# Kernel optimization log

Measured on AMD Instinct MI355X. Metric: run time of the kernel, lower is better.

The kernel has to match this reference:

```python
import jax, jax.numpy as jnp
import numpy as np

INPUT_DIM = 512
N_TREES = 64
TREE_DEPTH = 3
N_LEAVES = 2 ** TREE_DEPTH      # 8
N_INTERNAL = 2 ** TREE_DEPTH - 1  # 7
PPT = N_INTERNAL * (INPUT_DIM + 1) + N_LEAVES * 2  # params per tree = 3607
BATCH = 65536


def setup_inputs() -> dict:
    key = jax.random.key(0)
    k1, k2, k3 = jax.random.split(key, 3)
    x = jax.random.normal(k1, (BATCH, INPUT_DIM), dtype=jnp.float32)
    tree_params = jax.random.normal(k2, (1, N_TREES * PPT), dtype=jnp.float32)
    tree_weights = jax.random.normal(k3, (1, N_TREES), dtype=jnp.float32)
    return {"x": x, "tree_params": tree_params, "tree_weights": tree_weights}


def reference(x, tree_params, tree_weights):
    # Unpack all trees at once: [T, ppt]
    p = tree_params[0].reshape(N_TREES, PPT)
    split_w = p[:, : N_INTERNAL * INPUT_DIM].reshape(N_TREES, N_INTERNAL, INPUT_DIM)
    split_b = p[:, N_INTERNAL * INPUT_DIM : N_INTERNAL * (INPUT_DIM + 1)]  # [T, I]
    leaf_logits = p[:, N_INTERNAL * (INPUT_DIM + 1) :].reshape(N_TREES, N_LEAVES, 2)

    # decisions: [B, T, I]
    decisions = jax.nn.sigmoid(jnp.einsum('bd,tid->bti', x, split_w) + split_b[None])

    # Replicate the original indexing quirk: leaf_probs column j (a tree NODE index)
    # gets factor d_i if j == 2i+1 (and j < n_leaves), (1-d_i) if j == 2i+2.
    # Column 0 remains 1.0; each other column gets exactly one factor.
    cols = []
    for j in range(N_LEAVES):
        if j == 0:
            cols.append(jnp.ones_like(decisions[:, :, 0]))
        elif j % 2 == 1:
            i = (j - 1) // 2
            cols.append(decisions[:, :, i] if i < N_INTERNAL else jnp.ones_like(decisions[:, :, 0]))
        else:
            i = (j - 2) // 2
            cols.append(1.0 - decisions[:, :, i] if i < N_INTERNAL else jnp.ones_like(decisions[:, :, 0]))
    leaf_probs = jnp.stack(cols, axis=-1)  # [B, T, L]
    leaf_probs = leaf_probs / (leaf_probs.sum(axis=-1, keepdims=True) + 1e-8)

    leaf_dist = jax.nn.softmax(leaf_logits, axis=-1)  # [T, L, 2]
    tree_out = jnp.einsum('btl,tlc->btc', leaf_probs, leaf_dist)  # [B, T, 2]
    return jnp.einsum('btc,t->bc', tree_out, tree_weights[0])  # [B, 2]
```

## Files before the change

kernel.cpp:

```cpp
#include <hip/hip_runtime.h>
#include <stdint.h>


#define KDIM 512
#define PPT 3607
#define NP 8
#define EPI_S 260
#define E_OFF 65536
#define P_OFF 98816
#define P_S 34
#define AB_OFF 103168
#define LDS_BYTES 105728

typedef _Float16 f16x8 __attribute__((ext_vector_type(8)));
typedef float f32x4 __attribute__((ext_vector_type(4)));

__global__ __launch_bounds__(128) void prep_kernel(const float* __restrict__ p,
                                                   const float* __restrict__ tw,
                                                   _Float16* __restrict__ Wh,
                                                   float* __restrict__ biasN,
                                                   float* __restrict__ AB) {
    const int c = blockIdx.x;
    const int t = c >> 2, i = c & 3;
    const float* wsrc = p + t * PPT + i * KDIM;
    for (int k = threadIdx.x; k < KDIM; k += 128)
        Wh[c * KDIM + k] = (_Float16)wsrc[k];
    if (threadIdx.x == 0)
        biasN[c] = p[t * PPT + 7 * KDIM + i];
    if (threadIdx.x == 64 && c < 64) {
        const int tt = c;
        const float* lg = p + tt * PPT + 7 * 513;
        const float w = tw[tt];
        float ld[8][2];
#pragma unroll
        for (int j = 0; j < 8; ++j) {
            float a = lg[2 * j], b = lg[2 * j + 1];
            float m = fmaxf(a, b);
            float e0 = expf(a - m), e1 = expf(b - m);
            float s = e0 + e1;
            ld[j][0] = e0 / s; ld[j][1] = e1 / s;
        }
        float* o = AB + tt * 10;
#pragma unroll
        for (int cc = 0; cc < 2; ++cc) {
            o[0 + cc] = w * (ld[0][cc] + ld[2][cc] + ld[4][cc] + ld[6][cc]);
            o[2 + cc] = w * (ld[1][cc] - ld[2][cc]);
            o[4 + cc] = w * (ld[3][cc] - ld[4][cc]);
            o[6 + cc] = w * (ld[5][cc] - ld[6][cc]);
            o[8 + cc] = w * (ld[7][cc]);
        }
    }
}

__device__ __forceinline__ f16x8 cvt8(float4 a, float4 b) {
    f16x8 h;
    h[0] = (_Float16)a.x; h[1] = (_Float16)a.y; h[2] = (_Float16)a.z; h[3] = (_Float16)a.w;
    h[4] = (_Float16)b.x; h[5] = (_Float16)b.y; h[6] = (_Float16)b.z; h[7] = (_Float16)b.w;
    return h;
}

__global__ __launch_bounds__(512, 2) void main_kernel(const float* __restrict__ X,
                                                      const _Float16* __restrict__ Wh,
                                                      const float* __restrict__ biasN,
                                                      const float* __restrict__ ABg,
                                                      float* __restrict__ out) {
    extern __shared__ char smem[];
    const int tid = threadIdx.x;
    const int lane = tid & 63;
    const int wn = tid >> 6;
    const int r15 = lane & 15;
    const int hi = lane >> 4;
    const int gr0 = blockIdx.x * 256;

    {
        float* abl = (float*)(smem + AB_OFF);
        for (int i = tid; i < 640; i += 512) abl[i] = ABg[i];
    }

    f16x8 Wf[16][2];
#pragma unroll
    for (int s = 0; s < 16; ++s)
#pragma unroll
        for (int ct = 0; ct < 2; ++ct)
            Wf[s][ct] = *(const f16x8*)&Wh[(size_t)(wn * 32 + ct * 16 + r15) * KDIM + s * 32 + hi * 8];

    float bl[2];
#pragma unroll
    for (int ct = 0; ct < 2; ++ct) bl[ct] = biasN[wn * 32 + ct * 16 + r15];

    int srow[4], ldw[4];
#pragma unroll
    for (int i = 0; i < 4; ++i) {
        int chunk = i * 512 + tid;
        int row = chunk >> 6, g = chunk & 63;
        srow[i] = chunk * 8;
        ldw[i] = row * 1024 + ((g ^ (row & 15)) << 4);
    }

    const int aoff0 = r15 * 1024;
    const int aoff1 = (16 + r15) * 1024;

    const float* Xblk = X + (size_t)gr0 * KDIM;
    float4 xr[8];

#pragma unroll
    for (int i = 0; i < 4; ++i) {
        xr[2 * i]     = *(const float4*)(Xblk + srow[i]);
        xr[2 * i + 1] = *(const float4*)(Xblk + srow[i] + 4);
    }

    for (int p = 0; p < NP; ++p) {
        char* xb = smem + (p & 1) * 32768;
#pragma unroll
        for (int i = 0; i < 4; ++i)
            *(f16x8*)(xb + ldw[i]) = cvt8(xr[2 * i], xr[2 * i + 1]);
        if (p + 1 < NP) {
            const float* Xp = Xblk + (size_t)(p + 1) * 32 * KDIM;
#pragma unroll
            for (int i = 0; i < 4; ++i) {
                xr[2 * i]     = *(const float4*)(Xp + srow[i]);
                xr[2 * i + 1] = *(const float4*)(Xp + srow[i] + 4);
            }
        }
        asm volatile("s_waitcnt lgkmcnt(0)" ::: "memory");
        __builtin_amdgcn_s_barrier();

        f32x4 acc[2][2];
#pragma unroll
        for (int rt = 0; rt < 2; ++rt)
#pragma unroll
            for (int ct = 0; ct < 2; ++ct)
                acc[rt][ct] = (f32x4){0.f, 0.f, 0.f, 0.f};
#pragma unroll
        for (int s = 0; s < 16; ++s) {
            const int go = ((s * 4 + hi) ^ r15) << 4;
            f16x8 a0 = *(const f16x8*)(xb + aoff0 + go);
            f16x8 a1 = *(const f16x8*)(xb + aoff1 + go);
            acc[0][0] = __builtin_amdgcn_mfma_f32_16x16x32_f16(a0, Wf[s][0], acc[0][0], 0, 0, 0);
            acc[0][1] = __builtin_amdgcn_mfma_f32_16x16x32_f16(a0, Wf[s][1], acc[0][1], 0, 0, 0);
            acc[1][0] = __builtin_amdgcn_mfma_f32_16x16x32_f16(a1, Wf[s][0], acc[1][0], 0, 0, 0);
            acc[1][1] = __builtin_amdgcn_mfma_f32_16x16x32_f16(a1, Wf[s][1], acc[1][1], 0, 0, 0);
        }

        float* Ef = (float*)(smem + E_OFF);
#pragma unroll
        for (int rt = 0; rt < 2; ++rt)
#pragma unroll
            for (int ct = 0; ct < 2; ++ct) {
                const int col = wn * 32 + ct * 16 + r15;
#pragma unroll
                for (int reg = 0; reg < 4; ++reg) {
                    const int row = rt * 16 + hi * 4 + reg;
                    float z = acc[rt][ct][reg] + bl[ct];
                    Ef[row * EPI_S + col] = __builtin_amdgcn_rcpf(1.f + __expf(-z));
                }
            }
        asm volatile("s_waitcnt lgkmcnt(0)" ::: "memory");
        __builtin_amdgcn_s_barrier();
        {
            const float* abl = (const float*)(smem + AB_OFF);
            float* Pf = (float*)(smem + P_OFF);
            const int row = tid >> 4, tg = tid & 15;
            float s0 = 0.f, s1 = 0.f;
#pragma unroll
            for (int j = 0; j < 4; ++j) {
                const int t = tg * 4 + j;
                float4 dv = *(const float4*)&Ef[row * EPI_S + t * 4];
                const float* abt = &abl[t * 10];
                float inv = __builtin_amdgcn_rcpf(4.f + dv.w + 1e-8f);
                s0 += (abt[0] + dv.x * abt[2] + dv.y * abt[4] + dv.z * abt[6] + dv.w * abt[8]) * inv;
                s1 += (abt[1] + dv.x * abt[3] + dv.y * abt[5] + dv.z * abt[7] + dv.w * abt[9]) * inv;
            }
            Pf[row * P_S + tg * 2 + 0] = s0;
            Pf[row * P_S + tg * 2 + 1] = s1;
        }
        asm volatile("s_waitcnt lgkmcnt(0)" ::: "memory");
        __builtin_amdgcn_s_barrier();
        if (tid < 64) {
            const float* Pf = (const float*)(smem + P_OFF);
            const int row = tid >> 1, c = tid & 1;
            float s = 0.f;
#pragma unroll
            for (int tg = 0; tg < 16; ++tg) s += Pf[row * P_S + tg * 2 + c];
            out[(size_t)(gr0 + p * 32 + row) * 2 + c] = s;
        }
    }
}

extern "C" void kernel_launch(void* const* d_in, const int* in_sizes, int n_in,
                              void* d_out, int out_size, void* d_ws, size_t ws_size,
                              hipStream_t stream) {
    const float* x  = (const float*)d_in[0];
    const float* tp = (const float*)d_in[1];
    const float* tw = (const float*)d_in[2];
    float* out = (float*)d_out;

    _Float16* Wh = (_Float16*)d_ws;
    float* biasN = (float*)((char*)d_ws + 262144);
    float* AB    = (float*)((char*)d_ws + 263168);

    (void)hipFuncSetAttribute((const void*)reinterpret_cast<const void*>(&main_kernel),
                              hipFuncAttributeMaxDynamicSharedMemorySize, LDS_BYTES);

    prep_kernel<<<256, 128, 0, stream>>>(tp, tw, Wh, biasN, AB);
    main_kernel<<<256, 512, LDS_BYTES, stream>>>(x, Wh, biasN, AB, out);
}
```

Before: 47.62 us.

## Restructure GEMM into K-streamed 128x256 block tiles with async weight staging

Instead of holding all weights in registers and streaming 32-row X panels, each block now computes a 128-row by 256-column tile by looping over K in 16-wide steps. Weights are staged through a triple-buffered LDS ring via global_load_lds, and X goes through a double-buffered fp16 LDS tile. The grid doubles to 512 blocks with a smaller LDS footprint, aiming for higher occupancy and better latency hiding. The cost is 32 barriers per block, use of the smaller 16x16x16 MFMA, and weights re-read from global memory by every block.

Result: slower. 51.27 us (+7.7%).

```diff
diff --git a/kernel.cpp b/kernel.cpp
--- a/kernel.cpp
+++ b/kernel.cpp
@@ -4,16 +4,10 @@
 
 #define KDIM 512
 #define PPT 3607
-#define NP 8
-#define EPI_S 260
-#define E_OFF 65536
-#define P_OFF 98816
-#define P_S 34
-#define AB_OFF 103168
-#define LDS_BYTES 105728
-
-typedef _Float16 f16x8 __attribute__((ext_vector_type(8)));
+
+typedef _Float16 f16x4 __attribute__((ext_vector_type(4)));
 typedef float f32x4 __attribute__((ext_vector_type(4)));
+
 
 __global__ __launch_bounds__(128) void prep_kernel(const float* __restrict__ p,
                                                    const float* __restrict__ tw,
@@ -52,14 +46,28 @@
     }
 }
 
-__device__ __forceinline__ f16x8 cvt8(float4 a, float4 b) {
-    f16x8 h;
-    h[0] = (_Float16)a.x; h[1] = (_Float16)a.y; h[2] = (_Float16)a.z; h[3] = (_Float16)a.w;
-    h[4] = (_Float16)b.x; h[5] = (_Float16)b.y; h[6] = (_Float16)b.z; h[7] = (_Float16)b.w;
+#define XB_STRIDE 5120
+#define WB0 10240
+#define WB_STRIDE 8192
+#define EPI_S 260
+#define P_OFF 66560
+#define P_S 18
+#define AB_OFF 71168
+#define LDS_BYTES 73728
+
+__device__ __forceinline__ void gll16(const void* g, void* l) {
+    __builtin_amdgcn_global_load_lds((const __attribute__((address_space(1))) uint32_t*)g,
+                                     (__attribute__((address_space(3))) uint32_t*)l, 16, 0, 0);
+}
+
+__device__ __forceinline__ f16x4 cvt4(float4 a) {
+    f16x4 h;
+    h[0] = (_Float16)a.x; h[1] = (_Float16)a.y;
+    h[2] = (_Float16)a.z; h[3] = (_Float16)a.w;
     return h;
 }
 
-__global__ __launch_bounds__(512, 2) void main_kernel(const float* __restrict__ X,
+__global__ __launch_bounds__(512, 4) void main_kernel(const float* __restrict__ X,
                                                       const _Float16* __restrict__ Wh,
                                                       const float* __restrict__ biasN,
                                                       const float* __restrict__ ABg,
@@ -67,104 +75,119 @@
     extern __shared__ char smem[];
     const int tid = threadIdx.x;
     const int lane = tid & 63;
-    const int wn = tid >> 6;
+    const int w = tid >> 6;
+    const int wm = w >> 2;
+    const int wn = w & 3;
     const int r15 = lane & 15;
     const int hi = lane >> 4;
-    const int gr0 = blockIdx.x * 256;
+    const int gr0 = blockIdx.x * 128;
 
     {
         float* abl = (float*)(smem + AB_OFF);
         for (int i = tid; i < 640; i += 512) abl[i] = ABg[i];
     }
-
-    f16x8 Wf[16][2];
-#pragma unroll
-    for (int s = 0; s < 16; ++s)
-#pragma unroll
-        for (int ct = 0; ct < 2; ++ct)
-            Wf[s][ct] = *(const f16x8*)&Wh[(size_t)(wn * 32 + ct * 16 + r15) * KDIM + s * 32 + hi * 8];
-
-    float bl[2];
-#pragma unroll
-    for (int ct = 0; ct < 2; ++ct) bl[ct] = biasN[wn * 32 + ct * 16 + r15];
-
-    int srow[4], ldw[4];
-#pragma unroll
-    for (int i = 0; i < 4; ++i) {
-        int chunk = i * 512 + tid;
-        int row = chunk >> 6, g = chunk & 63;
-        srow[i] = chunk * 8;
-        ldw[i] = row * 1024 + ((g ^ (row & 15)) << 4);
-    }
-
-    const int aoff0 = r15 * 1024;
-    const int aoff1 = (16 + r15) * 1024;
-
-    const float* Xblk = X + (size_t)gr0 * KDIM;
-    float4 xr[8];
-
-#pragma unroll
-    for (int i = 0; i < 4; ++i) {
-        xr[2 * i]     = *(const float4*)(Xblk + srow[i]);
-        xr[2 * i + 1] = *(const float4*)(Xblk + srow[i] + 4);
-    }
-
-    for (int p = 0; p < NP; ++p) {
-        char* xb = smem + (p & 1) * 32768;
-#pragma unroll
-        for (int i = 0; i < 4; ++i)
-            *(f16x8*)(xb + ldw[i]) = cvt8(xr[2 * i], xr[2 * i + 1]);
-        if (p + 1 < NP) {
-            const float* Xp = Xblk + (size_t)(p + 1) * 32 * KDIM;
-#pragma unroll
-            for (int i = 0; i < 4; ++i) {
-                xr[2 * i]     = *(const float4*)(Xp + srow[i]);
-                xr[2 * i + 1] = *(const float4*)(Xp + srow[i] + 4);
-            }
-        }
+    asm volatile("s_waitcnt vmcnt(0)" ::: "memory");
+
+    const int xrow = tid >> 2, xg = tid & 3;
+    const float* Xp = X + (size_t)(gr0 + xrow) * KDIM + xg * 4;
+    const int xw = xrow * 40 + xg * 8;
+
+    const int wc = tid >> 1, wgr = tid & 1;
+    const _Float16* Wp = Wh + (size_t)wc * KDIM + (((wgr ^ ((wc >> 2) & 1))) << 3);
+    const int ww = tid * 16;
+
+    const int aoff = (wm * 64 + r15) * 40 + hi * 8;
+    int boff[4];
+#pragma unroll
+    for (int ct = 0; ct < 4; ++ct) {
+        int col = wn * 64 + ct * 16 + r15;
+        boff[ct] = col * 32 + (((hi >> 1) ^ ((col >> 2) & 1)) << 4) + ((hi & 1) << 3);
+    }
+
+    f32x4 acc[4][4];
+#pragma unroll
+    for (int rt = 0; rt < 4; ++rt)
+#pragma unroll
+        for (int ct = 0; ct < 4; ++ct)
+            acc[rt][ct] = (f32x4){0.f, 0.f, 0.f, 0.f};
+
+    float4 xr[3];
+
+    {
+        float4 x0 = *(const float4*)(Xp + 0);
+        gll16(Wp + 0 * 16, smem + WB0 + 0 * WB_STRIDE + ww);
+        xr[1] = *(const float4*)(Xp + 1 * 16);
+        gll16(Wp + 1 * 16, smem + WB0 + 1 * WB_STRIDE + ww);
+        xr[2] = *(const float4*)(Xp + 2 * 16);
+        asm volatile("s_waitcnt vmcnt(4)" ::: "memory");
+        *(f16x4*)(smem + xw) = cvt4(x0);
+    }
+
+#pragma unroll
+    for (int kt = 0; kt < 32; ++kt) {
+        if (kt <= 29)      asm volatile("s_waitcnt vmcnt(2)" ::: "memory");
+        else if (kt == 30) asm volatile("s_waitcnt vmcnt(1)" ::: "memory");
+        else               asm volatile("s_waitcnt vmcnt(0)" ::: "memory");
         asm volatile("s_waitcnt lgkmcnt(0)" ::: "memory");
         __builtin_amdgcn_s_barrier();
-
-        f32x4 acc[2][2];
-#pragma unroll
-        for (int rt = 0; rt < 2; ++rt)
-#pragma unroll
-            for (int ct = 0; ct < 2; ++ct)
-                acc[rt][ct] = (f32x4){0.f, 0.f, 0.f, 0.f};
-#pragma unroll
-        for (int s = 0; s < 16; ++s) {
-            const int go = ((s * 4 + hi) ^ r15) << 4;
-            f16x8 a0 = *(const f16x8*)(xb + aoff0 + go);
-            f16x8 a1 = *(const f16x8*)(xb + aoff1 + go);
-            acc[0][0] = __builtin_amdgcn_mfma_f32_16x16x32_f16(a0, Wf[s][0], acc[0][0], 0, 0, 0);
-            acc[0][1] = __builtin_amdgcn_mfma_f32_16x16x32_f16(a0, Wf[s][1], acc[0][1], 0, 0, 0);
-            acc[1][0] = __builtin_amdgcn_mfma_f32_16x16x32_f16(a1, Wf[s][0], acc[1][0], 0, 0, 0);
-            acc[1][1] = __builtin_amdgcn_mfma_f32_16x16x32_f16(a1, Wf[s][1], acc[1][1], 0, 0, 0);
-        }
-
-        float* Ef = (float*)(smem + E_OFF);
-#pragma unroll
-        for (int rt = 0; rt < 2; ++rt)
-#pragma unroll
-            for (int ct = 0; ct < 2; ++ct) {
-                const int col = wn * 32 + ct * 16 + r15;
-#pragma unroll
-                for (int reg = 0; reg < 4; ++reg) {
-                    const int row = rt * 16 + hi * 4 + reg;
-                    float z = acc[rt][ct][reg] + bl[ct];
-                    Ef[row * EPI_S + col] = __builtin_amdgcn_rcpf(1.f + __expf(-z));
+        if (kt <= 29)
+            gll16(Wp + (size_t)(kt + 2) * 16,
+                  smem + WB0 + ((kt + 2) % 3) * WB_STRIDE + ww);
+        if (kt <= 30)
+            *(f16x4*)(smem + ((kt + 1) & 1) * XB_STRIDE + xw) = cvt4(xr[(kt + 1) % 3]);
+        if (kt <= 28)
+            xr[kt % 3] = *(const float4*)(Xp + (size_t)(kt + 3) * 16);
+        {
+            const char* xb = smem + (kt & 1) * XB_STRIDE;
+            const char* wb = smem + WB0 + (kt % 3) * WB_STRIDE;
+            f16x4 bfr[4];
+#pragma unroll
+            for (int ct = 0; ct < 4; ++ct)
+                bfr[ct] = *(const f16x4*)(wb + boff[ct]);
+#pragma unroll
+            for (int rt = 0; rt < 4; ++rt) {
+                f16x4 a = *(const f16x4*)(xb + aoff + rt * 640);
+#pragma unroll
+                for (int ct = 0; ct < 4; ++ct)
+                    acc[rt][ct] = __builtin_amdgcn_mfma_f32_16x16x16f16(a, bfr[ct], acc[rt][ct], 0, 0, 0);
+            }
+        }
+    }
+
+    asm volatile("s_waitcnt lgkmcnt(0)" ::: "memory");
+    __builtin_amdgcn_s_barrier();
+
+    float bl[4];
+#pragma unroll
+    for (int ct = 0; ct < 4; ++ct) bl[ct] = biasN[wn * 64 + ct * 16 + r15];
+
+    for (int p = 0; p < 2; ++p) {
+        if (wm == p) {
+            float* Ef = (float*)smem;
+#pragma unroll
+            for (int rt = 0; rt < 4; ++rt)
+#pragma unroll
+                for (int ct = 0; ct < 4; ++ct) {
+                    const int col = wn * 64 + ct * 16 + r15;
+#pragma unroll
+                    for (int reg = 0; reg < 4; ++reg) {
+                        const int row = rt * 16 + hi * 4 + reg;
+                        float z = acc[rt][ct][reg] + bl[ct];
+                        Ef[row * EPI_S + col] = __builtin_amdgcn_rcpf(1.f + __expf(-z));
+                    }
                 }
-            }
+        }
         asm volatile("s_waitcnt lgkmcnt(0)" ::: "memory");
         __builtin_amdgcn_s_barrier();
         {
+            const float* Ef = (const float*)smem;
             const float* abl = (const float*)(smem + AB_OFF);
             float* Pf = (float*)(smem + P_OFF);
-            const int row = tid >> 4, tg = tid & 15;
+            const int row = tid >> 3, tg = tid & 7;
             float s0 = 0.f, s1 = 0.f;
 #pragma unroll
-            for (int j = 0; j < 4; ++j) {
-                const int t = tg * 4 + j;
+            for (int j = 0; j < 8; ++j) {
+                const int t = tg * 8 + ((j + tg) & 7);
                 float4 dv = *(const float4*)&Ef[row * EPI_S + t * 4];
                 const float* abt = &abl[t * 10];
                 float inv = __builtin_amdgcn_rcpf(4.f + dv.w + 1e-8f);
@@ -176,13 +199,17 @@
         }
         asm volatile("s_waitcnt lgkmcnt(0)" ::: "memory");
         __builtin_amdgcn_s_barrier();
-        if (tid < 64) {
+        if (tid < 128) {
             const float* Pf = (const float*)(smem + P_OFF);
             const int row = tid >> 1, c = tid & 1;
             float s = 0.f;
 #pragma unroll
-            for (int tg = 0; tg < 16; ++tg) s += Pf[row * P_S + tg * 2 + c];
-            out[(size_t)(gr0 + p * 32 + row) * 2 + c] = s;
+            for (int g = 0; g < 8; ++g) s += Pf[row * P_S + g * 2 + c];
+            out[(size_t)(gr0 + p * 64 + row) * 2 + c] = s;
+        }
+        if (p == 0) {
+            asm volatile("s_waitcnt lgkmcnt(0)" ::: "memory");
+            __builtin_amdgcn_s_barrier();
         }
     }
 }
@@ -203,5 +230,5 @@
                               hipFuncAttributeMaxDynamicSharedMemorySize, LDS_BYTES);
 
     prep_kernel<<<256, 128, 0, stream>>>(tp, tw, Wh, biasN, AB);
-    main_kernel<<<256, 512, LDS_BYTES, stream>>>(x, Wh, biasN, AB, out);
-}
+    main_kernel<<<512, 512, LDS_BYTES, stream>>>(x, Wh, biasN, AB, out);
+}
```

## Stream weights per K-step with smaller row tiles and more blocks

Applied to the files above, without the earlier changes.

The main kernel previously kept all of its weights resident in registers and walked 256 rows in 32-row chunks. It now processes 64 rows per block, streams the weight fragments and x slices along K with a rotating register prefetch, and double-buffers small fp16 x tiles in LDS. The cut in LDS and registers allows 4 blocks per CU and a 1024-block grid, aiming for more occupancy and better latency hiding. In exchange, the weights are reread from global or L2 by every block, and there is a barrier on each K-step.

New measurement: 56.34 us. 1.18x slower.

```diff
diff --git a/kernel.cpp b/kernel.cpp
--- a/kernel.cpp
+++ b/kernel.cpp
@@ -4,16 +4,11 @@
 
 #define KDIM 512
 #define PPT 3607
-#define NP 8
-#define EPI_S 260
-#define E_OFF 65536
-#define P_OFF 98816
-#define P_S 34
-#define AB_OFF 103168
-#define LDS_BYTES 105728
-
+
+typedef _Float16 f16x4 __attribute__((ext_vector_type(4)));
 typedef _Float16 f16x8 __attribute__((ext_vector_type(8)));
 typedef float f32x4 __attribute__((ext_vector_type(4)));
+
 
 __global__ __launch_bounds__(128) void prep_kernel(const float* __restrict__ p,
                                                    const float* __restrict__ tw,
@@ -52,14 +47,22 @@
     }
 }
 
-__device__ __forceinline__ f16x8 cvt8(float4 a, float4 b) {
-    f16x8 h;
-    h[0] = (_Float16)a.x; h[1] = (_Float16)a.y; h[2] = (_Float16)a.z; h[3] = (_Float16)a.w;
-    h[4] = (_Float16)b.x; h[5] = (_Float16)b.y; h[6] = (_Float16)b.z; h[7] = (_Float16)b.w;
+#define XB_STRIDE 5120
+#define ROWB 80
+#define EPI_S 260
+#define AB_OFF 33280
+#define P_OFF 35840
+#define P_S 34
+#define LDS_BYTES 40192
+
+__device__ __forceinline__ f16x4 cvt4(float4 a) {
+    f16x4 h;
+    h[0] = (_Float16)a.x; h[1] = (_Float16)a.y;
+    h[2] = (_Float16)a.z; h[3] = (_Float16)a.w;
     return h;
 }
 
-__global__ __launch_bounds__(512, 2) void main_kernel(const float* __restrict__ X,
+__global__ __launch_bounds__(512, 4) void main_kernel(const float* __restrict__ X,
                                                       const _Float16* __restrict__ Wh,
                                                       const float* __restrict__ biasN,
                                                       const float* __restrict__ ABg,
@@ -67,94 +70,91 @@
     extern __shared__ char smem[];
     const int tid = threadIdx.x;
     const int lane = tid & 63;
-    const int wn = tid >> 6;
+    const int w = tid >> 6;
     const int r15 = lane & 15;
     const int hi = lane >> 4;
-    const int gr0 = blockIdx.x * 256;
+    const int gr0 = blockIdx.x * 64;
 
     {
         float* abl = (float*)(smem + AB_OFF);
         for (int i = tid; i < 640; i += 512) abl[i] = ABg[i];
     }
 
-    f16x8 Wf[16][2];
-#pragma unroll
-    for (int s = 0; s < 16; ++s)
+    const int xrow = tid >> 3, xq = tid & 7;
+    const float* Xp = X + (size_t)(gr0 + xrow) * KDIM + xq * 4;
+    const int xw = xrow * ROWB + ((((xq >> 1) ^ (xrow & 3))) << 4) + ((xq & 1) << 3);
+
+    const _Float16* Wc0 = Wh + (size_t)(w * 32 + r15) * KDIM + hi * 8;
+    const _Float16* Wc1 = Wh + (size_t)(w * 32 + 16 + r15) * KDIM + hi * 8;
+
+    float bl[2];
+    bl[0] = biasN[w * 32 + r15];
+    bl[1] = biasN[w * 32 + 16 + r15];
+
+    const int aoff = r15 * ROWB + ((hi ^ (r15 & 3)) << 4);
+
+    f32x4 acc[4][2];
+#pragma unroll
+    for (int rt = 0; rt < 4; ++rt)
 #pragma unroll
         for (int ct = 0; ct < 2; ++ct)
-            Wf[s][ct] = *(const f16x8*)&Wh[(size_t)(wn * 32 + ct * 16 + r15) * KDIM + s * 32 + hi * 8];
-
-    float bl[2];
-#pragma unroll
-    for (int ct = 0; ct < 2; ++ct) bl[ct] = biasN[wn * 32 + ct * 16 + r15];
-
-    int srow[4], ldw[4];
-#pragma unroll
-    for (int i = 0; i < 4; ++i) {
-        int chunk = i * 512 + tid;
-        int row = chunk >> 6, g = chunk & 63;
-        srow[i] = chunk * 8;
-        ldw[i] = row * 1024 + ((g ^ (row & 15)) << 4);
-    }
-
-    const int aoff0 = r15 * 1024;
-    const int aoff1 = (16 + r15) * 1024;
-
-    const float* Xblk = X + (size_t)gr0 * KDIM;
-    float4 xr[8];
-
-#pragma unroll
-    for (int i = 0; i < 4; ++i) {
-        xr[2 * i]     = *(const float4*)(Xblk + srow[i]);
-        xr[2 * i + 1] = *(const float4*)(Xblk + srow[i] + 4);
-    }
-
-    for (int p = 0; p < NP; ++p) {
-        char* xb = smem + (p & 1) * 32768;
-#pragma unroll
-        for (int i = 0; i < 4; ++i)
-            *(f16x8*)(xb + ldw[i]) = cvt8(xr[2 * i], xr[2 * i + 1]);
-        if (p + 1 < NP) {
-            const float* Xp = Xblk + (size_t)(p + 1) * 32 * KDIM;
-#pragma unroll
-            for (int i = 0; i < 4; ++i) {
-                xr[2 * i]     = *(const float4*)(Xp + srow[i]);
-                xr[2 * i + 1] = *(const float4*)(Xp + srow[i] + 4);
+            acc[rt][ct] = (f32x4){0.f, 0.f, 0.f, 0.f};
+
+    float4 xr[4];
+    f16x8 Wf[3][2];
+
+    {
+        float4 x0 = *(const float4*)(Xp);
+        Wf[0][0] = *(const f16x8*)(Wc0);
+        Wf[0][1] = *(const f16x8*)(Wc1);
+        xr[1] = *(const float4*)(Xp + 32);
+        Wf[1][0] = *(const f16x8*)(Wc0 + 32);
+        Wf[1][1] = *(const f16x8*)(Wc1 + 32);
+        xr[2] = *(const float4*)(Xp + 64);
+        *(f16x4*)(smem + xw) = cvt4(x0);
+    }
+    asm volatile("s_waitcnt lgkmcnt(0)" ::: "memory");
+    __builtin_amdgcn_s_barrier();
+
+#pragma unroll
+    for (int kt = 0; kt < 16; ++kt) {
+        if (kt <= 12)
+            xr[(kt + 3) & 3] = *(const float4*)(Xp + (size_t)(kt + 3) * 32);
+        if (kt <= 13) {
+            Wf[(kt + 2) % 3][0] = *(const f16x8*)(Wc0 + (size_t)(kt + 2) * 32);
+            Wf[(kt + 2) % 3][1] = *(const f16x8*)(Wc1 + (size_t)(kt + 2) * 32);
+        }
+        if (kt <= 14)
+            *(f16x4*)(smem + ((kt + 1) & 1) * XB_STRIDE + xw) = cvt4(xr[(kt + 1) & 3]);
+        {
+            const char* xb = smem + (kt & 1) * XB_STRIDE;
+#pragma unroll
+            for (int rt = 0; rt < 4; ++rt) {
+                f16x8 a = *(const f16x8*)(xb + rt * 1280 + aoff);
+                acc[rt][0] = __builtin_amdgcn_mfma_f32_16x16x32_f16(a, Wf[kt % 3][0], acc[rt][0], 0, 0, 0);
+                acc[rt][1] = __builtin_amdgcn_mfma_f32_16x16x32_f16(a, Wf[kt % 3][1], acc[rt][1], 0, 0, 0);
             }
         }
         asm volatile("s_waitcnt lgkmcnt(0)" ::: "memory");
         __builtin_amdgcn_s_barrier();
-
-        f32x4 acc[2][2];
-#pragma unroll
-        for (int rt = 0; rt < 2; ++rt)
-#pragma unroll
-            for (int ct = 0; ct < 2; ++ct)
-                acc[rt][ct] = (f32x4){0.f, 0.f, 0.f, 0.f};
-#pragma unroll
-        for (int s = 0; s < 16; ++s) {
-            const int go = ((s * 4 + hi) ^ r15) << 4;
-            f16x8 a0 = *(const f16x8*)(xb + aoff0 + go);
-            f16x8 a1 = *(const f16x8*)(xb + aoff1 + go);
-            acc[0][0] = __builtin_amdgcn_mfma_f32_16x16x32_f16(a0, Wf[s][0], acc[0][0], 0, 0, 0);
-            acc[0][1] = __builtin_amdgcn_mfma_f32_16x16x32_f16(a0, Wf[s][1], acc[0][1], 0, 0, 0);
-            acc[1][0] = __builtin_amdgcn_mfma_f32_16x16x32_f16(a1, Wf[s][0], acc[1][0], 0, 0, 0);
-            acc[1][1] = __builtin_amdgcn_mfma_f32_16x16x32_f16(a1, Wf[s][1], acc[1][1], 0, 0, 0);
-        }
-
-        float* Ef = (float*)(smem + E_OFF);
-#pragma unroll
-        for (int rt = 0; rt < 2; ++rt)
+    }
+
+    for (int p = 0; p < 2; ++p) {
+        float* Ef = (float*)smem;
+#pragma unroll
+        for (int rt2 = 0; rt2 < 2; ++rt2) {
+            const int rt = p * 2 + rt2;
 #pragma unroll
             for (int ct = 0; ct < 2; ++ct) {
-                const int col = wn * 32 + ct * 16 + r15;
+                const int col = w * 32 + ct * 16 + r15;
 #pragma unroll
                 for (int reg = 0; reg < 4; ++reg) {
-                    const int row = rt * 16 + hi * 4 + reg;
+                    const int rowl = rt2 * 16 + hi * 4 + reg;
                     float z = acc[rt][ct][reg] + bl[ct];
-                    Ef[row * EPI_S + col] = __builtin_amdgcn_rcpf(1.f + __expf(-z));
+                    Ef[rowl * EPI_S + col] = __builtin_amdgcn_rcpf(1.f + __expf(-z));
                 }
             }
+        }
         asm volatile("s_waitcnt lgkmcnt(0)" ::: "memory");
         __builtin_amdgcn_s_barrier();
         {
@@ -164,7 +164,7 @@
             float s0 = 0.f, s1 = 0.f;
 #pragma unroll
             for (int j = 0; j < 4; ++j) {
-                const int t = tg * 4 + j;
+                const int t = tg * 4 + ((j + tg) & 3);
                 float4 dv = *(const float4*)&Ef[row * EPI_S + t * 4];
                 const float* abt = &abl[t * 10];
                 float inv = __builtin_amdgcn_rcpf(4.f + dv.w + 1e-8f);
@@ -203,5 +203,5 @@
                               hipFuncAttributeMaxDynamicSharedMemorySize, LDS_BYTES);
 
     prep_kernel<<<256, 128, 0, stream>>>(tp, tw, Wh, biasN, AB);
-    main_kernel<<<256, 512, LDS_BYTES, stream>>>(x, Wh, biasN, AB, out);
-}
+    main_kernel<<<1024, 512, LDS_BYTES, stream>>>(x, Wh, biasN, AB, out);
+}
```

## Split main kernel into many small 32-row blocks with streamed weight loads

Applied to the files above, without the earlier changes.

Replaces the persistent 256-block kernel, which looped over 8 row panels with a register-resident weight slice and a double-buffered X tile, with 2048 blocks of 256 threads that each handle a single 32-row panel. Each wave now covers 64 output columns and streams its fp16 weights from global/L2 memory with a two-stage register prefetch across the K loop. X is loaded with nontemporal loads directly into swizzled LDS, and the epilogue staggers tree indices across threads to reduce LDS bank conflicts. LDS use shrinks so more blocks fit per CU, but weights are now re-read from cache by every block, and there is no overlap between X loading and MFMA work inside a block.

Result: slower. 124.3 us (+161.0%).

```diff
diff --git a/kernel.cpp b/kernel.cpp
--- a/kernel.cpp
+++ b/kernel.cpp
@@ -4,16 +4,10 @@
 
 #define KDIM 512
 #define PPT 3607
-#define NP 8
-#define EPI_S 260
-#define E_OFF 65536
-#define P_OFF 98816
-#define P_S 34
-#define AB_OFF 103168
-#define LDS_BYTES 105728
 
 typedef _Float16 f16x8 __attribute__((ext_vector_type(8)));
 typedef float f32x4 __attribute__((ext_vector_type(4)));
+
 
 __global__ __launch_bounds__(128) void prep_kernel(const float* __restrict__ p,
                                                    const float* __restrict__ tw,
@@ -52,14 +46,20 @@
     }
 }
 
-__device__ __forceinline__ f16x8 cvt8(float4 a, float4 b) {
+#define EPI_S 260
+#define AB_OFF 33280
+#define P_OFF 35840
+#define P_S 18
+#define LDS_BYTES 38144
+
+__device__ __forceinline__ f16x8 cvt8(f32x4 a, f32x4 b) {
     f16x8 h;
     h[0] = (_Float16)a.x; h[1] = (_Float16)a.y; h[2] = (_Float16)a.z; h[3] = (_Float16)a.w;
     h[4] = (_Float16)b.x; h[5] = (_Float16)b.y; h[6] = (_Float16)b.z; h[7] = (_Float16)b.w;
     return h;
 }
 
-__global__ __launch_bounds__(512, 2) void main_kernel(const float* __restrict__ X,
+__global__ __launch_bounds__(256, 4) void main_kernel(const float* __restrict__ X,
                                                       const _Float16* __restrict__ Wh,
                                                       const float* __restrict__ biasN,
                                                       const float* __restrict__ ABg,
@@ -67,87 +67,79 @@
     extern __shared__ char smem[];
     const int tid = threadIdx.x;
     const int lane = tid & 63;
-    const int wn = tid >> 6;
+    const int wv = tid >> 6;
     const int r15 = lane & 15;
     const int hi = lane >> 4;
-    const int gr0 = blockIdx.x * 256;
+    const int gr0 = blockIdx.x * 32;
 
     {
         float* abl = (float*)(smem + AB_OFF);
-        for (int i = tid; i < 640; i += 512) abl[i] = ABg[i];
+        for (int i = tid; i < 640; i += 256) abl[i] = ABg[i];
     }
 
-    f16x8 Wf[16][2];
+    {
+        const int row = tid >> 3, q = tid & 7;
+        const float* Xr = X + (size_t)(gr0 + row) * KDIM + q * 64;
+        char* xb = smem + row * 1024;
 #pragma unroll
-    for (int s = 0; s < 16; ++s)
-#pragma unroll
-        for (int ct = 0; ct < 2; ++ct)
-            Wf[s][ct] = *(const f16x8*)&Wh[(size_t)(wn * 32 + ct * 16 + r15) * KDIM + s * 32 + hi * 8];
-
-    float bl[2];
-#pragma unroll
-    for (int ct = 0; ct < 2; ++ct) bl[ct] = biasN[wn * 32 + ct * 16 + r15];
-
-    int srow[4], ldw[4];
-#pragma unroll
-    for (int i = 0; i < 4; ++i) {
-        int chunk = i * 512 + tid;
-        int row = chunk >> 6, g = chunk & 63;
-        srow[i] = chunk * 8;
-        ldw[i] = row * 1024 + ((g ^ (row & 15)) << 4);
+        for (int j = 0; j < 8; ++j) {
+            const int g = q * 8 + j;
+            f32x4 a = __builtin_nontemporal_load((const f32x4*)(Xr + j * 8));
+            f32x4 b = __builtin_nontemporal_load((const f32x4*)(Xr + j * 8 + 4));
+            *(f16x8*)(xb + ((g ^ (row & 15)) << 4)) = cvt8(a, b);
+        }
     }
 
-    const int aoff0 = r15 * 1024;
-    const int aoff1 = (16 + r15) * 1024;
+    const _Float16* Wbase = Wh + (size_t)(wv * 64 + r15) * KDIM + hi * 8;
 
-    const float* Xblk = X + (size_t)gr0 * KDIM;
-    float4 xr[8];
+    f32x4 acc[2][4];
+#pragma unroll
+    for (int rt = 0; rt < 2; ++rt)
+#pragma unroll
+        for (int ct = 0; ct < 4; ++ct)
+            acc[rt][ct] = (f32x4){0.f, 0.f, 0.f, 0.f};
+
+    f16x8 Wf[2][4];
+#pragma unroll
+    for (int ct = 0; ct < 4; ++ct)
+        Wf[0][ct] = *(const f16x8*)(Wbase + (size_t)ct * 16 * KDIM);
+
+    __syncthreads();
+
+    const char* xb0 = smem + r15 * 1024;
+    const char* xb1 = smem + (16 + r15) * 1024;
 
 #pragma unroll
-    for (int i = 0; i < 4; ++i) {
-        xr[2 * i]     = *(const float4*)(Xblk + srow[i]);
-        xr[2 * i + 1] = *(const float4*)(Xblk + srow[i] + 4);
+    for (int s = 0; s < 16; ++s) {
+        if (s < 15) {
+#pragma unroll
+            for (int ct = 0; ct < 4; ++ct)
+                Wf[(s + 1) & 1][ct] =
+                    *(const f16x8*)(Wbase + (size_t)ct * 16 * KDIM + (s + 1) * 32);
+        }
+        const int go = (((s * 4 + hi) ^ r15) << 4);
+        f16x8 a0 = *(const f16x8*)(xb0 + go);
+        f16x8 a1 = *(const f16x8*)(xb1 + go);
+#pragma unroll
+        for (int ct = 0; ct < 4; ++ct) {
+            acc[0][ct] = __builtin_amdgcn_mfma_f32_16x16x32_f16(a0, Wf[s & 1][ct], acc[0][ct], 0, 0, 0);
+            acc[1][ct] = __builtin_amdgcn_mfma_f32_16x16x32_f16(a1, Wf[s & 1][ct], acc[1][ct], 0, 0, 0);
+        }
     }
 
-    for (int p = 0; p < NP; ++p) {
-        char* xb = smem + (p & 1) * 32768;
+    __syncthreads();
+
+    float bl[4];
 #pragma unroll
-        for (int i = 0; i < 4; ++i)
-            *(f16x8*)(xb + ldw[i]) = cvt8(xr[2 * i], xr[2 * i + 1]);
-        if (p + 1 < NP) {
-            const float* Xp = Xblk + (size_t)(p + 1) * 32 * KDIM;
-#pragma unroll
-            for (int i = 0; i < 4; ++i) {
-                xr[2 * i]     = *(const float4*)(Xp + srow[i]);
-                xr[2 * i + 1] = *(const float4*)(Xp + srow[i] + 4);
-            }
-        }
-        asm volatile("s_waitcnt lgkmcnt(0)" ::: "memory");
-        __builtin_amdgcn_s_barrier();
+    for (int ct = 0; ct < 4; ++ct) bl[ct] = biasN[wv * 64 + ct * 16 + r15];
 
-        f32x4 acc[2][2];
+    {
+        float* Ef = (float*)smem;
 #pragma unroll
         for (int rt = 0; rt < 2; ++rt)
 #pragma unroll
-            for (int ct = 0; ct < 2; ++ct)
-                acc[rt][ct] = (f32x4){0.f, 0.f, 0.f, 0.f};
-#pragma unroll
-        for (int s = 0; s < 16; ++s) {
-            const int go = ((s * 4 + hi) ^ r15) << 4;
-            f16x8 a0 = *(const f16x8*)(xb + aoff0 + go);
-            f16x8 a1 = *(const f16x8*)(xb + aoff1 + go);
-            acc[0][0] = __builtin_amdgcn_mfma_f32_16x16x32_f16(a0, Wf[s][0], acc[0][0], 0, 0, 0);
-            acc[0][1] = __builtin_amdgcn_mfma_f32_16x16x32_f16(a0, Wf[s][1], acc[0][1], 0, 0, 0);
-            acc[1][0] = __builtin_amdgcn_mfma_f32_16x16x32_f16(a1, Wf[s][0], acc[1][0], 0, 0, 0);
-            acc[1][1] = __builtin_amdgcn_mfma_f32_16x16x32_f16(a1, Wf[s][1], acc[1][1], 0, 0, 0);
-        }
-
-        float* Ef = (float*)(smem + E_OFF);
-#pragma unroll
-        for (int rt = 0; rt < 2; ++rt)
-#pragma unroll
-            for (int ct = 0; ct < 2; ++ct) {
-                const int col = wn * 32 + ct * 16 + r15;
+            for (int ct = 0; ct < 4; ++ct) {
+                const int col = wv * 64 + ct * 16 + r15;
 #pragma unroll
                 for (int reg = 0; reg < 4; ++reg) {
                     const int row = rt * 16 + hi * 4 + reg;
@@ -155,35 +147,34 @@
                     Ef[row * EPI_S + col] = __builtin_amdgcn_rcpf(1.f + __expf(-z));
                 }
             }
-        asm volatile("s_waitcnt lgkmcnt(0)" ::: "memory");
-        __builtin_amdgcn_s_barrier();
-        {
-            const float* abl = (const float*)(smem + AB_OFF);
-            float* Pf = (float*)(smem + P_OFF);
-            const int row = tid >> 4, tg = tid & 15;
-            float s0 = 0.f, s1 = 0.f;
+    }
+    __syncthreads();
+    {
+        const float* Ef = (const float*)smem;
+        const float* abl = (const float*)(smem + AB_OFF);
+        float* Pf = (float*)(smem + P_OFF);
+        const int row = tid >> 3, tg = tid & 7;
+        float s0 = 0.f, s1 = 0.f;
 #pragma unroll
-            for (int j = 0; j < 4; ++j) {
-                const int t = tg * 4 + j;
-                float4 dv = *(const float4*)&Ef[row * EPI_S + t * 4];
-                const float* abt = &abl[t * 10];
-                float inv = __builtin_amdgcn_rcpf(4.f + dv.w + 1e-8f);
-                s0 += (abt[0] + dv.x * abt[2] + dv.y * abt[4] + dv.z * abt[6] + dv.w * abt[8]) * inv;
-                s1 += (abt[1] + dv.x * abt[3] + dv.y * abt[5] + dv.z * abt[7] + dv.w * abt[9]) * inv;
-            }
-            Pf[row * P_S + tg * 2 + 0] = s0;
-            Pf[row * P_S + tg * 2 + 1] = s1;
+        for (int j = 0; j < 8; ++j) {
+            const int t = tg * 8 + ((j + tg) & 7);
+            float4 dv = *(const float4*)&Ef[row * EPI_S + t * 4];
+            const float* abt = &abl[t * 10];
+            float inv = __builtin_amdgcn_rcpf(4.f + dv.w + 1e-8f);
+            s0 += (abt[0] + dv.x * abt[2] + dv.y * abt[4] + dv.z * abt[6] + dv.w * abt[8]) * inv;
+            s1 += (abt[1] + dv.x * abt[3] + dv.y * abt[5] + dv.z * abt[7] + dv.w * abt[9]) * inv;
         }
-        asm volatile("s_waitcnt lgkmcnt(0)" ::: "memory");
-        __builtin_amdgcn_s_barrier();
-        if (tid < 64) {
-            const float* Pf = (const float*)(smem + P_OFF);
-            const int row = tid >> 1, c = tid & 1;
-            float s = 0.f;
+        Pf[row * P_S + tg * 2 + 0] = s0;
+        Pf[row * P_S + tg * 2 + 1] = s1;
+    }
+    __syncthreads();
+    if (tid < 64) {
+        const float* Pf = (const float*)(smem + P_OFF);
+        const int row = tid >> 1, c = tid & 1;
+        float s = 0.f;
 #pragma unroll
-            for (int tg = 0; tg < 16; ++tg) s += Pf[row * P_S + tg * 2 + c];
-            out[(size_t)(gr0 + p * 32 + row) * 2 + c] = s;
-        }
+        for (int tg = 0; tg < 8; ++tg) s += Pf[row * P_S + tg * 2 + c];
+        out[(size_t)(gr0 + row) * 2 + c] = s;
     }
 }
 
@@ -203,5 +194,5 @@
                               hipFuncAttributeMaxDynamicSharedMemorySize, LDS_BYTES);
 
     prep_kernel<<<256, 128, 0, stream>>>(tp, tw, Wh, biasN, AB);
-    main_kernel<<<256, 512, LDS_BYTES, stream>>>(x, Wh, biasN, AB, out);
+    main_kernel<<<2048, 256, LDS_BYTES, stream>>>(x, Wh, biasN, AB, out);
 }
```
